# Kernel optimization log

Measured on AMD Instinct MI355X. Metric: run time of the kernel, lower is better.

## Reference

```python
import jax, jax.numpy as jnp
import numpy as np

HIDDEN_DIM = 2048
HEAD_NUM = 16
HEAD_DIM = HIDDEN_DIM // HEAD_NUM


def setup_inputs() -> dict:
    key = jax.random.key(0)
    ks = jax.random.split(key, 9)
    B, S, H = 2, 2048, HIDDEN_DIM
    scale = 1.0 / np.sqrt(H)
    X = jax.random.normal(ks[0], (B, S, H), dtype=jnp.float32)
    Wq = jax.random.normal(ks[1], (H, H), dtype=jnp.float32) * scale
    bq = jnp.zeros((H,), dtype=jnp.float32)
    Wk = jax.random.normal(ks[2], (H, H), dtype=jnp.float32) * scale
    bk = jnp.zeros((H,), dtype=jnp.float32)
    Wv = jax.random.normal(ks[3], (H, H), dtype=jnp.float32) * scale
    bv = jnp.zeros((H,), dtype=jnp.float32)
    Wo = jax.random.normal(ks[4], (H, H), dtype=jnp.float32) * scale
    bo = jnp.zeros((H,), dtype=jnp.float32)
    return {"X": X, "Wq": Wq, "bq": bq, "Wk": Wk, "bk": bk,
            "Wv": Wv, "bv": bv, "Wo": Wo, "bo": bo}


def reference(X, Wq, bq, Wk, bk, Wv, bv, Wo, bo):
    B, S, H = X.shape
    # QKV projections (nn.Linear applies x @ W.T + b; weights here stored as [in, out])
    Q = X @ Wq + bq
    K = X @ Wk + bk
    V = X @ Wv + bv
    # [B, heads, S, head_dim]
    q = Q.reshape(B, S, HEAD_NUM, HEAD_DIM).transpose(0, 2, 1, 3)
    k = K.reshape(B, S, HEAD_NUM, HEAD_DIM).transpose(0, 2, 1, 3)
    v = V.reshape(B, S, HEAD_NUM, HEAD_DIM).transpose(0, 2, 1, 3)
    scores = jnp.einsum('bhqd,bhkd->bhqk', q, k) / jnp.sqrt(jnp.float32(HEAD_DIM))
    attn = jax.nn.softmax(scores, axis=-1)  # dropout = identity in eval
    out = jnp.einsum('bhqk,bhkd->bhqd', attn, v)
    out = out.transpose(0, 2, 1, 3).reshape(B, S, H)
    return out @ Wo + bo
```

## Files before the change

kernel.cpp:

```cpp
#include <hip/hip_runtime.h>
#include <hip/hip_bf16.h>
#include <stdint.h>


#define Bc 2
#define Sc 2048
#define Hc 2048
#define NHc 16
#define Dc 128
#define Mc 4096

typedef unsigned short ushortT;
typedef float f32x4 __attribute__((ext_vector_type(4)));
typedef _Float16 f16x8 __attribute__((ext_vector_type(8)));

#define MFMAH(a, b, c) __builtin_amdgcn_mfma_f32_16x16x32_f16((a), (b), (c), 0, 0, 0)
#define MF_AB(a, b, c) MFMAH((a), (b), (c))
#define MF_BA(a, b, c) MFMAH((b), (a), (c))

static __device__ __forceinline__ ushortT f2h(float x) {
    _Float16 h = (_Float16)x;
    return __builtin_bit_cast(unsigned short, h);
}

static __device__ __forceinline__ void load_lds16(const ushortT* g, ushortT* l) {
    __builtin_amdgcn_global_load_lds(
        (__attribute__((address_space(1))) void*)(g),
        (__attribute__((address_space(3))) void*)(l), 16, 0, 0);
}

__global__ __launch_bounds__(256) void pack_a(
    const float* __restrict__ src, ushortT* __restrict__ dst)
{
    const int mt = blockIdx.x, kt = blockIdx.y;
    const int t = threadIdx.x;
    const int kq = t & 15;
    const int r0 = t >> 4;
    ushortT* tile = dst + ((size_t)(mt * 32 + kt)) * 8192;
#pragma unroll
    for (int rr = 0; rr < 8; ++rr) {
        const int row = r0 + rr * 16;
        const float4 v = *(const float4*)(src + (size_t)(mt * 128 + row) * Hc + kt * 64 + kq * 4);
        _Float16 h[4] = {(_Float16)v.x, (_Float16)v.y, (_Float16)v.z, (_Float16)v.w};
        const int gid = kq >> 1, halfg = kq & 1;
        const int gp = gid ^ (row & 7);
        *(uint2*)(tile + (size_t)row * 64 + gp * 8 + halfg * 4) = *(uint2*)h;
    }
}

__global__ __launch_bounds__(256) void pack_b(
    const float* __restrict__ W0, const float* __restrict__ W1,
    const float* __restrict__ W2, const float* __restrict__ W3,
    ushortT* __restrict__ dst)
{
    const int nt = blockIdx.x, kt = blockIdx.y, which = blockIdx.z;
    const float* W = (which == 0) ? W0 : (which == 1) ? W1 : (which == 2) ? W2 : W3;
    const int t = threadIdx.x;
    const int n = t & 127;
    const int g0 = (t >> 7) * 4;
    ushortT* tile = dst + (size_t)which * 4194304 + ((size_t)(nt * 32 + kt)) * 8192;
#pragma unroll
    for (int gi = 0; gi < 4; ++gi) {
        const int g = g0 + gi;
        _Float16 h[8];
#pragma unroll
        for (int j = 0; j < 8; ++j)
            h[j] = (_Float16)W[(size_t)(kt * 64 + g * 8 + j) * Hc + nt * 128 + n];
        const int gp = g ^ (n & 7);
        *(uint4*)(tile + (size_t)n * 64 + gp * 8) = *(uint4*)h;
    }
}

#define GEMM_PROLOGUE()                                                        \
    __shared__ __align__(16) ushortT As[8192], Bs[8192];                       \
    const int tid = threadIdx.x, wv_ = tid >> 6, lane = tid & 63;              \
    const int lane16 = lane & 15, quad = lane >> 4;                            \
    const int quad4 = quad * 4;                                                \
    const int wm = (wv_ & 1) * 64, wn = (wv_ >> 1) * 64;                       \
    int aoff[4][2], boff[4][2];                                                \
    _Pragma("unroll") for (int mi = 0; mi < 4; ++mi)                           \
        _Pragma("unroll") for (int kf = 0; kf < 2; ++kf) {                     \
            const int ra = wm + mi * 16 + lane16;                              \
            aoff[mi][kf] = ra * 64 + (((kf * 4 + quad) ^ (ra & 7)) << 3);      \
            const int rb = wn + mi * 16 + lane16;                              \
            boff[mi][kf] = rb * 64 + (((kf * 4 + quad) ^ (rb & 7)) << 3);      \
        }                                                                      \
    f32x4 acc[4][4];                                                           \
    _Pragma("unroll") for (int i = 0; i < 4; ++i)                              \
        _Pragma("unroll") for (int j = 0; j < 4; ++j) {                        \
            acc[i][j][0] = 0.f; acc[i][j][1] = 0.f;                            \
            acc[i][j][2] = 0.f; acc[i][j][3] = 0.f; }                          \
    ushortT* asd = &As[wv_ * 2048];                                            \
    ushortT* bsd = &Bs[wv_ * 2048];

#define GEMM_KLOOP(at, bt)                                                     \
    for (int kt2 = 0; kt2 < 32; ++kt2) {                                       \
        _Pragma("unroll") for (int i = 0; i < 4; ++i) {                        \
            load_lds16(at + i * 512 + lane * 8, asd + i * 512);                \
            load_lds16(bt + i * 512 + lane * 8, bsd + i * 512);                \
        }                                                                      \
        at += 8192; bt += 8192;                                                \
        __syncthreads();                                                       \
        _Pragma("unroll") for (int kf = 0; kf < 2; ++kf) {                     \
            f16x8 a[4], b[4];                                                  \
            _Pragma("unroll") for (int mi = 0; mi < 4; ++mi)                   \
                a[mi] = *(const f16x8*)&As[aoff[mi][kf]];                      \
            _Pragma("unroll") for (int nj = 0; nj < 4; ++nj)                   \
                b[nj] = *(const f16x8*)&Bs[boff[nj][kf]];                      \
            _Pragma("unroll") for (int nj = 0; nj < 4; ++nj)                   \
                _Pragma("unroll") for (int mi = 0; mi < 4; ++mi)               \
                    acc[mi][nj] = MFMAH(a[mi], b[nj], acc[mi][nj]);            \
        }                                                                      \
        __syncthreads();                                                       \
    }

#define G256_PROLOGUE()                                                        \
    __shared__ __align__(16) ushortT LA[2][2][8192];                           \
    __shared__ __align__(16) ushortT LB[2][2][8192];                           \
    const int tid = threadIdx.x, wv_ = tid >> 6, lane = tid & 63;              \
    const int lane16 = lane & 15, quad = lane >> 4, quad4 = (lane >> 4) * 4;   \
    const int wr = wv_ >> 2, wc = wv_ & 3;                                     \
    const ushortT* LAr = &LA[0][0][0] + wr * 8192;                             \
    const ushortT* LBr = &LB[0][0][0] + (wc >> 1) * 8192;                      \
    int oA[2][4][2], oB[4][2];                                                 \
    _Pragma("unroll") for (int h = 0; h < 2; ++h)                              \
        _Pragma("unroll") for (int mi = 0; mi < 4; ++mi)                       \
            _Pragma("unroll") for (int kf = 0; kf < 2; ++kf) {                 \
                const int r_ = h * 64 + mi * 16 + lane16;                      \
                oA[h][mi][kf] = r_ * 64 + (((kf * 4 + quad) ^ (r_ & 7)) << 3); \
            }                                                                  \
    _Pragma("unroll") for (int nj = 0; nj < 4; ++nj)                           \
        _Pragma("unroll") for (int kf = 0; kf < 2; ++kf) {                     \
            const int r_ = (wc & 1) * 64 + nj * 16 + lane16;                   \
            oB[nj][kf] = r_ * 64 + (((kf * 4 + quad) ^ (r_ & 7)) << 3);        \
        }                                                                      \
    f32x4 acc[8][4];                                                           \
    _Pragma("unroll") for (int i = 0; i < 8; ++i)                              \
        _Pragma("unroll") for (int j = 0; j < 4; ++j) {                        \
            acc[i][j][0] = 0.f; acc[i][j][1] = 0.f;                            \
            acc[i][j][2] = 0.f; acc[i][j][3] = 0.f; }

#define STAGE(SRC, STEP, DST) do {                                             \
    const ushortT* g_ = (SRC) + (size_t)(STEP) * 8192;                         \
    ushortT* l_ = (DST) + wv_ * 1024;                                          \
    load_lds16(g_, l_);                                                        \
    load_lds16(g_ + 512, l_ + 512);                                            \
} while (0)

#define RD_A(S, H)                                                             \
    _Pragma("unroll") for (int mi = 0; mi < 4; ++mi)                           \
        _Pragma("unroll") for (int kf = 0; kf < 2; ++kf)                       \
            a[mi][kf] = *(const f16x8*)&LAr[(S) * 16384 + oA[H][mi][kf]];

#define RD_B(S)                                                                \
    _Pragma("unroll") for (int nj = 0; nj < 4; ++nj)                           \
        _Pragma("unroll") for (int kf = 0; kf < 2; ++kf)                       \
            b[nj][kf] = *(const f16x8*)&LBr[(S) * 16384 + oB[nj][kf]];

#define QUAD(MIB, NJB, MF)                                                     \
    _Pragma("unroll") for (int kf = 0; kf < 2; ++kf)                           \
        _Pragma("unroll") for (int mi = 0; mi < 4; ++mi)                       \
            _Pragma("unroll") for (int nj = 0; nj < 2; ++nj)                   \
                acc[(MIB) + mi][(NJB) + nj] =                                  \
                    MF(a[mi][kf], b[(NJB) + nj][kf], acc[(MIB) + mi][(NJB) + nj]);

#define PRE_MFMA()                                                             \
    __builtin_amdgcn_s_barrier();                                              \
    __builtin_amdgcn_s_setprio(1);

#define POST_MFMA()                                                            \
    __builtin_amdgcn_s_setprio(0);                                             \
    __builtin_amdgcn_s_barrier();

#define VMC6() asm volatile("s_waitcnt vmcnt(6)" ::: "memory")

#define MINS(x) ((x) < 31 ? (x) : 31)

#define G256_MAIN(AB0, AB1, BB0, BB1, MF)                                      \
    const ushortT* sA0 = (AB0) + wv_ * 1024 + lane * 8;                        \
    const ushortT* sA1 = (AB1) + wv_ * 1024 + lane * 8;                        \
    const ushortT* sB0 = (BB0) + wv_ * 1024 + lane * 8;                        \
    const ushortT* sB1 = (BB1) + wv_ * 1024 + lane * 8;                        \
      \
    STAGE(sB0, 0, &LB[0][0][0]); STAGE(sB1, 0, &LB[0][1][0]);                  \
    STAGE(sA0, 0, &LA[0][0][0]); STAGE(sA1, 0, &LA[0][1][0]);                  \
    STAGE(sB0, 1, &LB[1][0][0]); STAGE(sB1, 1, &LB[1][1][0]);                  \
    STAGE(sA0, 1, &LA[1][0][0]);                                               \
    VMC6();                                                                    \
    __builtin_amdgcn_s_barrier();                                              \
    _Pragma("clang loop unroll(disable)")                                      \
    for (int t = 0; t < 32; t += 2) {                                          \
        f16x8 a[4][2], b[4][2];                                                \
                                \
        RD_A(0, 0); RD_B(0);                                                   \
        STAGE(sA1, t + 1, &LA[1][1][0]);                                       \
        PRE_MFMA(); QUAD(0, 0, MF); POST_MFMA();                               \
                                            \
        STAGE(sB0, MINS(t + 2), &LB[0][0][0]);                                 \
        PRE_MFMA(); QUAD(0, 2, MF); POST_MFMA();                               \
                                                       \
        RD_A(0, 1);                                                            \
        STAGE(sB1, MINS(t + 2), &LB[0][1][0]);                                 \
        PRE_MFMA(); QUAD(4, 2, MF); POST_MFMA();                               \
            \
        STAGE(sA0, MINS(t + 2), &LA[0][0][0]);                                 \
        VMC6();                                                                \
        PRE_MFMA(); QUAD(4, 0, MF); POST_MFMA();                               \
                                             \
        RD_A(1, 0); RD_B(1);                                                   \
        STAGE(sA1, MINS(t + 2), &LA[0][1][0]);                                 \
        PRE_MFMA(); QUAD(0, 0, MF); POST_MFMA();                               \
                                                                       \
        STAGE(sB0, MINS(t + 3), &LB[1][0][0]);                                 \
        PRE_MFMA(); QUAD(0, 2, MF); POST_MFMA();                               \
                                                                       \
        RD_A(1, 1);                                                            \
        STAGE(sB1, MINS(t + 3), &LB[1][1][0]);                                 \
        PRE_MFMA(); QUAD(4, 2, MF); POST_MFMA();                               \
                            \
        STAGE(sA0, MINS(t + 3), &LA[1][0][0]);                                 \
        VMC6();                                                                \
        PRE_MFMA(); QUAD(4, 0, MF); POST_MFMA();                               \
    }

__global__ __launch_bounds__(512, 2) void qkv_gemm256(
    const ushortT* __restrict__ Xp, const ushortT* __restrict__ Wall,
    const float* __restrict__ bq, const float* __restrict__ bk,
    const float* __restrict__ bv,
    ushortT* __restrict__ Qd, ushortT* __restrict__ Kd, ushortT* __restrict__ Vt)
{
    const int id = blockIdx.x;
    const int swz = (id & 7) * 48 + (id >> 3);
    const int mt = swz & 15;
    const int bn = swz >> 4;
    const int which = bn >> 3, bnw = bn & 7;
    const ushortT* Ab0 = Xp + (size_t)((2 * mt + 0) * 32) * 8192;
    const ushortT* Ab1 = Xp + (size_t)((2 * mt + 1) * 32) * 8192;
    const ushortT* Wp  = Wall + (size_t)which * 4194304;
    const ushortT* Bb0 = Wp + (size_t)((bnw * 2 + 0) * 32) * 8192;
    const ushortT* Bb1 = Wp + (size_t)((bnw * 2 + 1) * 32) * 8192;
    const float* bias = (which == 0) ? bq : (which == 1) ? bk : bv;

    G256_PROLOGUE();

    const float QS = 0.08838834764831845f * 1.4426950408889634f;

    if (which == 2) {
        G256_MAIN(Ab0, Ab1, Bb0, Bb1, MF_AB);
        asm volatile("s_waitcnt vmcnt(0)" ::: "memory");
#pragma unroll
        for (int nj = 0; nj < 4; ++nj) {
            const int colm = bnw * 256 + wc * 64 + nj * 16 + lane16;
            const float bb2 = bias[colm];
            const int dd = colm & 127;
            const int hh = colm >> 7;
#pragma unroll
            for (int mi = 0; mi < 8; ++mi) {
                const int m0 = mt * 256 + wr * 128 + mi * 16 + quad4;
                const int b = m0 >> 11, s0_ = m0 & 2047;
                const size_t bhb = (size_t)(b * NHc + hh) * (Sc * Dc);
                const int t2 = s0_ >> 6, sin0 = s0_ & 63;
                uint2 u;
                u.x = (uint32_t)f2h(acc[mi][nj][0] + bb2) |
                      ((uint32_t)f2h(acc[mi][nj][1] + bb2) << 16);
                u.y = (uint32_t)f2h(acc[mi][nj][2] + bb2) |
                      ((uint32_t)f2h(acc[mi][nj][3] + bb2) << 16);
                *(uint2*)&Vt[bhb + (size_t)t2 * 8192 + dd * 64 +
                             (((sin0 >> 3) ^ (dd & 7)) << 3) + (sin0 & 7)] = u;
            }
        }
    } else {
        G256_MAIN(Ab0, Ab1, Bb0, Bb1, MF_BA);
        asm volatile("s_waitcnt vmcnt(0)" ::: "memory");
#pragma unroll
        for (int nj = 0; nj < 4; ++nj) {
            const int col0 = bnw * 256 + wc * 64 + nj * 16 + quad4;
            const float4 bv4 = *(const float4*)&bias[col0];
            const int dd0 = col0 & 127;
            const int hh = col0 >> 7;
#pragma unroll
            for (int mi = 0; mi < 8; ++mi) {
                const int m = mt * 256 + wr * 128 + mi * 16 + lane16;
                const int b = m >> 11, s = m & 2047;
                const size_t bhb = (size_t)(b * NHc + hh) * (Sc * Dc);
                float v0 = acc[mi][nj][0] + bv4.x;
                float v1 = acc[mi][nj][1] + bv4.y;
                float v2 = acc[mi][nj][2] + bv4.z;
                float v3 = acc[mi][nj][3] + bv4.w;
                if (which == 0) {
                    uint2 u;
                    u.x = (uint32_t)f2h(v0 * QS) | ((uint32_t)f2h(v1 * QS) << 16);
                    u.y = (uint32_t)f2h(v2 * QS) | ((uint32_t)f2h(v3 * QS) << 16);
                    *(uint2*)&Qd[bhb + (size_t)s * Dc + dd0] = u;
                } else {
                    const int t2 = s >> 6, sin_ = s & 63;
                    uint2 u;
                    u.x = (uint32_t)f2h(v0) | ((uint32_t)f2h(v1) << 16);
                    u.y = (uint32_t)f2h(v2) | ((uint32_t)f2h(v3) << 16);
                    *(uint2*)&Kd[bhb + (size_t)t2 * 8192 + sin_ * 128 +
                                 (((dd0 >> 3) ^ (sin_ & 7)) << 3) + (dd0 & 7)] = u;
                }
            }
        }
    }
}

__global__ __launch_bounds__(128, 2) void attn(
    const ushortT* __restrict__ Qd, const ushortT* __restrict__ Kt,
    const ushortT* __restrict__ Vt, ushortT* __restrict__ AOp)
{
    const int id = blockIdx.x;
    const int slot = id >> 3;
    const int pair = (id & 7) + ((slot >> 5) << 3);
    const int qt = slot & 31;
    const int hh = pair & 15, bb = pair >> 4;

    const ushortT* Qp  = Qd + ((size_t)(bb * NHc + hh)) * Sc * Dc;
    const ushortT* Kbh = Kt + ((size_t)(bb * NHc + hh)) * Sc * Dc;
    const ushortT* Vbh = Vt + ((size_t)(bb * NHc + hh)) * Sc * Dc;

    __shared__ __align__(16) ushortT Ks[8192];
    __shared__ __align__(16) ushortT Vs[8192];
    __shared__ __align__(16) ushortT Pbuf[2][2048];

    const int tid = threadIdx.x, wv_ = tid >> 6, lane = tid & 63;
    const int lane16 = lane & 15, quad = lane >> 4;
    const int quad8 = quad * 8, quad4 = quad * 4;
    const int s0 = qt * 64 + wv_ * 32;

    f16x8 q[2][4];
#pragma unroll
    for (int nj = 0; nj < 2; ++nj)
#pragma unroll
        for (int kf = 0; kf < 4; ++kf)
            q[nj][kf] = *(const f16x8*)(Qp + (size_t)(s0 + nj * 16 + lane16) * Dc + kf * 32 + quad8);

    f32x4 o[8][2];
#pragma unroll
    for (int dj = 0; dj < 8; ++dj)
#pragma unroll
        for (int nj = 0; nj < 2; ++nj) { o[dj][nj][0] = 0.f; o[dj][nj][1] = 0.f; o[dj][nj][2] = 0.f; o[dj][nj][3] = 0.f; }

    float m_run[2] = {-1e30f, -1e30f}, l_run[2] = {0.f, 0.f};
    ushortT* Pw = Pbuf[wv_];

    for (int nt = 0; nt < 32; ++nt) {
        const ushortT* ktile = Kbh + (size_t)nt * 8192 + wv_ * 4096;
        const ushortT* vtile = Vbh + (size_t)nt * 8192 + wv_ * 4096;
#pragma unroll
        for (int i = 0; i < 8; ++i) {
            load_lds16(ktile + i * 512 + lane * 8, Ks + wv_ * 4096 + i * 512);
            load_lds16(vtile + i * 512 + lane * 8, Vs + wv_ * 4096 + i * 512);
        }
        __syncthreads();

        f32x4 sacc[4][2];
#pragma unroll
        for (int mi = 0; mi < 4; ++mi)
#pragma unroll
            for (int nj = 0; nj < 2; ++nj) { sacc[mi][nj][0] = 0.f; sacc[mi][nj][1] = 0.f; sacc[mi][nj][2] = 0.f; sacc[mi][nj][3] = 0.f; }
        __builtin_amdgcn_s_setprio(1);
#pragma unroll
        for (int kf = 0; kf < 4; ++kf) {
            f16x8 kb[4];
#pragma unroll
            for (int mi = 0; mi < 4; ++mi) {
                const int row = mi * 16 + lane16;
                kb[mi] = *(const f16x8*)&Ks[row * 128 + (((kf * 4 + quad) ^ (row & 7)) << 3)];
            }
#pragma unroll
            for (int mi = 0; mi < 4; ++mi)
#pragma unroll
                for (int nj = 0; nj < 2; ++nj)
                    sacc[mi][nj] = MFMAH(kb[mi], q[nj][kf], sacc[mi][nj]);
        }
        __builtin_amdgcn_s_setprio(0);

        float alpha_[2];
#pragma unroll
        for (int nj = 0; nj < 2; ++nj) {
            float mx = sacc[0][nj][0];
#pragma unroll
            for (int mi = 0; mi < 4; ++mi)
#pragma unroll
                for (int r = 0; r < 4; ++r) mx = fmaxf(mx, sacc[mi][nj][r]);
            mx = fmaxf(mx, __shfl_xor(mx, 16));
            mx = fmaxf(mx, __shfl_xor(mx, 32));
            const float mnew = fmaxf(m_run[nj], mx);
            alpha_[nj] = exp2f(m_run[nj] - mnew);
            m_run[nj] = mnew;
            float sum = 0.f;
#pragma unroll
            for (int mi = 0; mi < 4; ++mi)
#pragma unroll
                for (int r = 0; r < 4; ++r) {
                    const float p = exp2f(sacc[mi][nj][r] - mnew);
                    sacc[mi][nj][r] = p;
                    sum += p;
                }
            sum += __shfl_xor(sum, 16);
            sum += __shfl_xor(sum, 32);
            l_run[nj] = l_run[nj] * alpha_[nj] + sum;
            const int prow = nj * 16 + lane16;
#pragma unroll
            for (int mi = 0; mi < 4; ++mi) {
                uint2 u;
                u.x = (uint32_t)f2h(sacc[mi][nj][0]) | ((uint32_t)f2h(sacc[mi][nj][1]) << 16);
                u.y = (uint32_t)f2h(sacc[mi][nj][2]) | ((uint32_t)f2h(sacc[mi][nj][3]) << 16);
                const int g = mi * 2 + (quad >> 1);
                *(uint2*)&Pw[prow * 64 + ((g ^ (prow & 7)) << 3) + (quad & 1) * 4] = u;
            }
        }

        if (__ballot((alpha_[0] != 1.f) | (alpha_[1] != 1.f)) != 0ull) {
#pragma unroll
            for (int dj = 0; dj < 8; ++dj)
#pragma unroll
                for (int nj = 0; nj < 2; ++nj) {
                    const float av = alpha_[nj];
                    o[dj][nj][0] *= av; o[dj][nj][1] *= av;
                    o[dj][nj][2] *= av; o[dj][nj][3] *= av;
                }
        }

        __builtin_amdgcn_s_setprio(1);
#pragma unroll
        for (int kf2 = 0; kf2 < 2; ++kf2) {
            f16x8 pb[2];
#pragma unroll
            for (int nj = 0; nj < 2; ++nj) {
                const int row = nj * 16 + lane16;
                pb[nj] = *(const f16x8*)&Pw[row * 64 + (((kf2 * 4 + quad) ^ (row & 7)) << 3)];
            }
#pragma unroll
            for (int dj = 0; dj < 8; ++dj) {
                const int row = dj * 16 + lane16;
                const f16x8 vb = *(const f16x8*)&Vs[row * 64 + (((kf2 * 4 + quad) ^ (row & 7)) << 3)];
#pragma unroll
                for (int nj = 0; nj < 2; ++nj)
                    o[dj][nj] = MFMAH(vb, pb[nj], o[dj][nj]);
            }
        }
        __builtin_amdgcn_s_setprio(0);
        __syncthreads();
    }

#pragma unroll
    for (int nj = 0; nj < 2; ++nj) {
        const float inv = 1.f / l_run[nj];
        const int m = bb * Sc + qt * 64 + wv_ * 32 + nj * 16 + lane16;
        const int mtile = m >> 7, rin = m & 127;
#pragma unroll
        for (int dj = 0; dj < 8; ++dj) {
            const int ktile = hh * 2 + (dj >> 2);
            const int cin0 = (dj & 3) * 16 + quad4;
            const int g = cin0 >> 3, e0 = cin0 & 7;
            uint2 u;
            u.x = (uint32_t)f2h(o[dj][nj][0] * inv) | ((uint32_t)f2h(o[dj][nj][1] * inv) << 16);
            u.y = (uint32_t)f2h(o[dj][nj][2] * inv) | ((uint32_t)f2h(o[dj][nj][3] * inv) << 16);
            *(uint2*)&AOp[((size_t)(mtile * 32 + ktile)) * 8192 + rin * 64 +
                          ((g ^ (rin & 7)) << 3) + e0] = u;
        }
    }
}

__global__ __launch_bounds__(256) void out_gemm(
    const ushortT* __restrict__ AOp, const ushortT* __restrict__ Wop,
    const float* __restrict__ bo, float* __restrict__ out)
{
    const int nt = blockIdx.x;
    const int mt = blockIdx.y;

    GEMM_PROLOGUE();

    const ushortT* at = AOp + (size_t)(mt * 32) * 8192 + wv_ * 2048;
    const ushortT* bt = Wop + (size_t)(nt * 32) * 8192 + wv_ * 2048;
    GEMM_KLOOP(at, bt);

#pragma unroll
    for (int nj = 0; nj < 4; ++nj) {
        const int col = nt * 128 + wn + nj * 16 + lane16;
        const float bb = bo[col];
#pragma unroll
        for (int mi = 0; mi < 4; ++mi)
#pragma unroll
            for (int r = 0; r < 4; ++r) {
                const int m = mt * 128 + wm + mi * 16 + quad4 + r;
                out[(size_t)m * Hc + col] = acc[mi][nj][r] + bb;
            }
    }
}

extern "C" void kernel_launch(void* const* d_in, const int* in_sizes, int n_in,
                              void* d_out, int out_size, void* d_ws, size_t ws_size,
                              hipStream_t stream) {
    (void)in_sizes; (void)n_in; (void)out_size; (void)ws_size;

    const float* X  = (const float*)d_in[0];
    const float* Wq = (const float*)d_in[1];
    const float* bq = (const float*)d_in[2];
    const float* Wk = (const float*)d_in[3];
    const float* bk = (const float*)d_in[4];
    const float* Wv = (const float*)d_in[5];
    const float* bv = (const float*)d_in[6];
    const float* Wo = (const float*)d_in[7];
    const float* bo = (const float*)d_in[8];
    float* out = (float*)d_out;

    ushortT* ws = (ushortT*)d_ws;
    const size_t E = (size_t)Mc * Hc;
    const size_t WE = (size_t)Hc * Hc;
    ushortT* Xp   = ws;
    ushortT* Wall = Xp + E;
    ushortT* Qd   = Wall + 4 * WE;
    ushortT* Kd   = Qd + E;
    ushortT* Vtp  = Kd + E;
    ushortT* AOp  = Vtp + E;

    pack_a<<<dim3(32, 32), 256, 0, stream>>>(X, Xp);
    pack_b<<<dim3(16, 32, 4), 256, 0, stream>>>(Wq, Wk, Wv, Wo, Wall);
    qkv_gemm256<<<dim3(384), 512, 0, stream>>>(Xp, Wall, bq, bk, bv, Qd, Kd, Vtp);
    attn<<<dim3(1024), 128, 0, stream>>>(Qd, Kd, Vtp, AOp);
    out_gemm<<<dim3(16, 32), 256, 0, stream>>>(AOp, Wall + 3 * WE, bo, out);
}
```

Baseline: 450.8 us.

## Vectorize weight packing, split LDS fragment reads, and vectorize output stores

pack_b now loads float4 rows of W and transposes them in registers, replacing strided scalar loads. The 256-tile GEMM main loop splits A and B fragment reads into smaller pieces (a03/a47, b01/b23) spread across MFMA phases, with an added vmcnt(4) wait, so LDS reads interleave better with MFMAs. out_gemm swaps the MFMA operand order so each lane holds 4 consecutive columns and can write float4 stores and load the bias as a float4. The finer interleaving changes register pressure and wait placement, which could disturb the existing schedule.

```diff
diff --git a/kernel.cpp b/kernel.cpp
--- a/kernel.cpp
+++ b/kernel.cpp
@@ -56,18 +56,20 @@
     const int nt = blockIdx.x, kt = blockIdx.y, which = blockIdx.z;
     const float* W = (which == 0) ? W0 : (which == 1) ? W1 : (which == 2) ? W2 : W3;
     const int t = threadIdx.x;
-    const int n = t & 127;
-    const int g0 = (t >> 7) * 4;
+    const int n0 = (t & 31) * 4;
+    const int kg = t >> 5;
     ushortT* tile = dst + (size_t)which * 4194304 + ((size_t)(nt * 32 + kt)) * 8192;
-#pragma unroll
-    for (int gi = 0; gi < 4; ++gi) {
-        const int g = g0 + gi;
-        _Float16 h[8];
-#pragma unroll
-        for (int j = 0; j < 8; ++j)
-            h[j] = (_Float16)W[(size_t)(kt * 64 + g * 8 + j) * Hc + nt * 128 + n];
-        const int gp = g ^ (n & 7);
-        *(uint4*)(tile + (size_t)n * 64 + gp * 8) = *(uint4*)h;
+    _Float16 h[4][8];
+#pragma unroll
+    for (int j = 0; j < 8; ++j) {
+        const float4 v = *(const float4*)&W[(size_t)(kt * 64 + kg * 8 + j) * Hc + nt * 128 + n0];
+        h[0][j] = (_Float16)v.x; h[1][j] = (_Float16)v.y;
+        h[2][j] = (_Float16)v.z; h[3][j] = (_Float16)v.w;
+    }
+#pragma unroll
+    for (int i = 0; i < 4; ++i) {
+        const int n = n0 + i;
+        *(uint4*)(tile + (size_t)n * 64 + ((kg ^ (n & 7)) << 3)) = *(uint4*)h[i];
     }
 }
 
@@ -93,7 +95,7 @@
     ushortT* asd = &As[wv_ * 2048];                                            \
     ushortT* bsd = &Bs[wv_ * 2048];
 
-#define GEMM_KLOOP(at, bt)                                                     \
+#define GEMM_KLOOP(at, bt, MF)                                                 \
     for (int kt2 = 0; kt2 < 32; ++kt2) {                                       \
         _Pragma("unroll") for (int i = 0; i < 4; ++i) {                        \
             load_lds16(at + i * 512 + lane * 8, asd + i * 512);                \
@@ -109,7 +111,7 @@
                 b[nj] = *(const f16x8*)&Bs[boff[nj][kf]];                      \
             _Pragma("unroll") for (int nj = 0; nj < 4; ++nj)                   \
                 _Pragma("unroll") for (int mi = 0; mi < 4; ++mi)               \
-                    acc[mi][nj] = MFMAH(a[mi], b[nj], acc[mi][nj]);            \
+                    acc[mi][nj] = MF(a[mi], b[nj], acc[mi][nj]);               \
         }                                                                      \
         __syncthreads();                                                       \
     }
@@ -147,22 +149,32 @@
     load_lds16(g_ + 512, l_ + 512);                                            \
 } while (0)
 
-#define RD_A(S, H)                                                             \
+#define RD_A03(S)                                                              \
     _Pragma("unroll") for (int mi = 0; mi < 4; ++mi)                           \
         _Pragma("unroll") for (int kf = 0; kf < 2; ++kf)                       \
-            a[mi][kf] = *(const f16x8*)&LAr[(S) * 16384 + oA[H][mi][kf]];
-
-#define RD_B(S)                                                                \
-    _Pragma("unroll") for (int nj = 0; nj < 4; ++nj)                           \
+            a03[mi][kf] = *(const f16x8*)&LAr[(S) * 16384 + oA[0][mi][kf]];
+
+#define RD_A47(S)                                                              \
+    _Pragma("unroll") for (int mi = 0; mi < 4; ++mi)                           \
+        _Pragma("unroll") for (int kf = 0; kf < 2; ++kf)                       \
+            a47[mi][kf] = *(const f16x8*)&LAr[(S) * 16384 + oA[1][mi][kf]];
+
+#define RD_B01(S)                                                              \
+    _Pragma("unroll") for (int nj = 0; nj < 2; ++nj)                           \
         _Pragma("unroll") for (int kf = 0; kf < 2; ++kf)                       \
             b[nj][kf] = *(const f16x8*)&LBr[(S) * 16384 + oB[nj][kf]];
 
-#define QUAD(MIB, NJB, MF)                                                     \
+#define RD_B23(S)                                                              \
+    _Pragma("unroll") for (int nj = 2; nj < 4; ++nj)                           \
+        _Pragma("unroll") for (int kf = 0; kf < 2; ++kf)                       \
+            b[nj][kf] = *(const f16x8*)&LBr[(S) * 16384 + oB[nj][kf]];
+
+#define QUADQ(ARR, MIB, NJB, MF)                                               \
     _Pragma("unroll") for (int kf = 0; kf < 2; ++kf)                           \
         _Pragma("unroll") for (int mi = 0; mi < 4; ++mi)                       \
             _Pragma("unroll") for (int nj = 0; nj < 2; ++nj)                   \
                 acc[(MIB) + mi][(NJB) + nj] =                                  \
-                    MF(a[mi][kf], b[(NJB) + nj][kf], acc[(MIB) + mi][(NJB) + nj]);
+                    MF(ARR[mi][kf], b[(NJB) + nj][kf], acc[(MIB) + mi][(NJB) + nj]);
 
 #define PRE_MFMA()                                                             \
     __builtin_amdgcn_s_barrier();                                              \
@@ -173,6 +185,7 @@
     __builtin_amdgcn_s_barrier();
 
 #define VMC6() asm volatile("s_waitcnt vmcnt(6)" ::: "memory")
+#define VMC4() asm volatile("s_waitcnt vmcnt(4)" ::: "memory")
 
 #define MINS(x) ((x) < 31 ? (x) : 31)
 
@@ -190,37 +203,39 @@
     __builtin_amdgcn_s_barrier();                                              \
     _Pragma("clang loop unroll(disable)")                                      \
     for (int t = 0; t < 32; t += 2) {                                          \
-        f16x8 a[4][2], b[4][2];                                                \
-                                \
-        RD_A(0, 0); RD_B(0);                                                   \
+        f16x8 a03[4][2], a47[4][2], b[4][2];                                   \
+                                        \
+        RD_A03(0); RD_B01(0);                                                  \
         STAGE(sA1, t + 1, &LA[1][1][0]);                                       \
-        PRE_MFMA(); QUAD(0, 0, MF); POST_MFMA();                               \
-                                            \
+        PRE_MFMA(); QUADQ(a03, 0, 0, MF); POST_MFMA();                         \
+                                                       \
+        RD_B23(0);                                                             \
+        PRE_MFMA(); QUADQ(a03, 0, 2, MF); POST_MFMA();                         \
+                             \
+        RD_A47(0);                                                             \
         STAGE(sB0, MINS(t + 2), &LB[0][0][0]);                                 \
-        PRE_MFMA(); QUAD(0, 2, MF); POST_MFMA();                               \
-                                                       \
-        RD_A(0, 1);                                                            \
+        PRE_MFMA(); QUADQ(a47, 4, 2, MF); POST_MFMA();                         \
+              \
         STAGE(sB1, MINS(t + 2), &LB[0][1][0]);                                 \
-        PRE_MFMA(); QUAD(4, 2, MF); POST_MFMA();                               \
-            \
+        VMC4();                                                                \
+        PRE_MFMA(); QUADQ(a47, 4, 0, MF); POST_MFMA();                         \
+                        \
+        RD_A03(1); RD_B01(1);                                                  \
         STAGE(sA0, MINS(t + 2), &LA[0][0][0]);                                 \
-        VMC6();                                                                \
-        PRE_MFMA(); QUAD(4, 0, MF); POST_MFMA();                               \
-                                             \
-        RD_A(1, 0); RD_B(1);                                                   \
         STAGE(sA1, MINS(t + 2), &LA[0][1][0]);                                 \
-        PRE_MFMA(); QUAD(0, 0, MF); POST_MFMA();                               \
+        PRE_MFMA(); QUADQ(a03, 0, 0, MF); POST_MFMA();                         \
                                                                        \
+        RD_B23(1);                                                             \
+        PRE_MFMA(); QUADQ(a03, 0, 2, MF); POST_MFMA();                         \
+                                                                       \
+        RD_A47(1);                                                             \
         STAGE(sB0, MINS(t + 3), &LB[1][0][0]);                                 \
-        PRE_MFMA(); QUAD(0, 2, MF); POST_MFMA();                               \
-                                                                       \
-        RD_A(1, 1);                                                            \
+        PRE_MFMA(); QUADQ(a47, 4, 2, MF); POST_MFMA();                         \
+        \
         STAGE(sB1, MINS(t + 3), &LB[1][1][0]);                                 \
-        PRE_MFMA(); QUAD(4, 2, MF); POST_MFMA();                               \
-                            \
         STAGE(sA0, MINS(t + 3), &LA[1][0][0]);                                 \
         VMC6();                                                                \
-        PRE_MFMA(); QUAD(4, 0, MF); POST_MFMA();                               \
+        PRE_MFMA(); QUADQ(a47, 4, 0, MF); POST_MFMA();                         \
     }
 
 __global__ __launch_bounds__(512, 2) void qkv_gemm256(
@@ -475,19 +490,22 @@
 
     const ushortT* at = AOp + (size_t)(mt * 32) * 8192 + wv_ * 2048;
     const ushortT* bt = Wop + (size_t)(nt * 32) * 8192 + wv_ * 2048;
-    GEMM_KLOOP(at, bt);
+    GEMM_KLOOP(at, bt, MF_BA);
 
 #pragma unroll
     for (int nj = 0; nj < 4; ++nj) {
-        const int col = nt * 128 + wn + nj * 16 + lane16;
-        const float bb = bo[col];
-#pragma unroll
-        for (int mi = 0; mi < 4; ++mi)
-#pragma unroll
-            for (int r = 0; r < 4; ++r) {
-                const int m = mt * 128 + wm + mi * 16 + quad4 + r;
-                out[(size_t)m * Hc + col] = acc[mi][nj][r] + bb;
-            }
+        const int col0 = nt * 128 + wn + nj * 16 + quad4;
+        const float4 bv4 = *(const float4*)&bo[col0];
+#pragma unroll
+        for (int mi = 0; mi < 4; ++mi) {
+            const int m = mt * 128 + wm + mi * 16 + lane16;
+            float4 v;
+            v.x = acc[mi][nj][0] + bv4.x;
+            v.y = acc[mi][nj][1] + bv4.y;
+            v.z = acc[mi][nj][2] + bv4.z;
+            v.w = acc[mi][nj][3] + bv4.w;
+            *(float4*)&out[(size_t)m * Hc + col0] = v;
+        }
     }
 }
 
```

Result: faster. 430.2 us (-4.6%).
